# Kernel optimization log

Hardware: AMD Instinct MI355X
Metric: run time of the kernel (lower is better)

## Reference

```python
import jax, jax.numpy as jnp
import numpy as np


def setup_inputs() -> dict:
    key = jax.random.key(0)
    k1, k2, k3 = jax.random.split(key, 3)
    N, E, C_in, C_out = 100000, 3200000, 256, 64
    x = jax.random.normal(k1, (N, C_in), dtype=jnp.float32)
    edge_index = jax.random.randint(k2, (2, E), 0, N, dtype=jnp.int64)
    W = jax.random.normal(k3, (C_in, C_out), dtype=jnp.float32) * (1.0 / np.sqrt(C_in))
    b = jnp.zeros((C_out,), dtype=jnp.float32)
    return {"x": x, "edge_index": edge_index, "W": W, "b": b}


def reference(x, edge_index, W, b):
    # GCNConv: out = D^{-1/2} (A + I) D^{-1/2} (X W) + b
    N = x.shape[0]
    loop = jnp.arange(N, dtype=edge_index.dtype)
    src = jnp.concatenate([edge_index[0], loop])  # [E+N]
    dst = jnp.concatenate([edge_index[1], loop])  # [E+N]
    # degree (with self-loops) on destination nodes, unit edge weights
    deg = jax.ops.segment_sum(jnp.ones_like(dst, dtype=x.dtype), dst, num_segments=N)
    dinv = jnp.where(deg > 0, jax.lax.rsqrt(deg), 0.0)
    norm = dinv[src] * dinv[dst]  # [E+N]
    h = x @ W  # [N, C_out] dense projection before message passing
    msg = h[src] * norm[:, None]  # gather + scale
    out = jax.ops.segment_sum(msg, dst, num_segments=N)  # scatter-add
    return out + b
```

## Files before the change

### kernel.cpp

```cpp
#include <hip/hip_runtime.h>
#include <hip/hip_bf16.h>

#define CIN 256
#define COUT 64
#define WPAD 264
#define BSHIFT 7
#define NPB 128
#define NWG 1024

typedef __attribute__((ext_vector_type(8))) short short8;
typedef __attribute__((ext_vector_type(4))) float floatx4;

static __device__ __forceinline__ unsigned int fbits(float f) {
    return __builtin_bit_cast(unsigned int, f);
}
static __device__ __forceinline__ float bbits(unsigned int u) {
    return __builtin_bit_cast(float, u);
}
static __device__ __forceinline__ unsigned short f2bf(float f) {
    unsigned u = fbits(f);
    return (unsigned short)((u + 0x7FFFu + ((u >> 16) & 1u)) >> 16);
}
static __device__ __forceinline__ float bf2f(unsigned short h) {
    return bbits(((unsigned)h) << 16);
}

union U8 { short8 s; unsigned int u[4]; };
static __device__ __forceinline__ void split8(floatx4 a0, floatx4 a1,
                                              short8& hi, short8& lo) {
    float f[8] = {a0[0], a0[1], a0[2], a0[3], a1[0], a1[1], a1[2], a1[3]};
    U8 H, L;
#pragma unroll
    for (int j = 0; j < 4; ++j) {
        unsigned u0 = fbits(f[2 * j]);
        unsigned u1 = fbits(f[2 * j + 1]);
        H.u[j] = __builtin_amdgcn_perm(u1, u0, 0x07060302u);
        float r0 = f[2 * j] - bbits(u0 & 0xFFFF0000u);
        float r1 = f[2 * j + 1] - bbits(u1 & 0xFFFF0000u);
        L.u[j] = __builtin_amdgcn_perm(fbits(r1), fbits(r0), 0x07060302u);
    }
    hi = H.s;
    lo = L.s;
}

__global__ __launch_bounds__(256) void k1_bucket_hist(const int* __restrict__ dst,
                                                      int* __restrict__ H,
                                                      int E, int chunk, int nbuck) {
    __shared__ int cnt[1024];
    for (int i = threadIdx.x; i < nbuck; i += 256) cnt[i] = 0;
    __syncthreads();
    const int g = blockIdx.x;
    const int e0 = g * chunk;
    const int e1 = min(E, e0 + chunk);
    for (int e = e0 + threadIdx.x; e < e1; e += 256)
        atomicAdd(&cnt[dst[e] >> BSHIFT], 1);
    __syncthreads();
    for (int i = threadIdx.x; i < nbuck; i += 256) H[i * NWG + g] = cnt[i];
}

__global__ __launch_bounds__(1024) void scan_a(const int* __restrict__ in,
                                               int* __restrict__ out,
                                               int* __restrict__ bsums, int n) {
    __shared__ int sm[1024];
    int i = blockIdx.x * 1024 + threadIdx.x;
    int v = (i < n) ? in[i] : 0;
    sm[threadIdx.x] = v;
    __syncthreads();
    for (int off = 1; off < 1024; off <<= 1) {
        int t = (threadIdx.x >= off) ? sm[threadIdx.x - off] : 0;
        __syncthreads();
        sm[threadIdx.x] += t;
        __syncthreads();
    }
    if (i < n) out[i] = sm[threadIdx.x] - v;
    if (threadIdx.x == 1023) bsums[blockIdx.x] = sm[1023];
}

__global__ __launch_bounds__(1024) void scan_b(const int* __restrict__ bsums,
                                               int* __restrict__ boffs, int NB) {
    __shared__ int sm[1024];
    int v = (threadIdx.x < NB) ? bsums[threadIdx.x] : 0;
    sm[threadIdx.x] = v;
    __syncthreads();
    for (int off = 1; off < 1024; off <<= 1) {
        int t = (threadIdx.x >= off) ? sm[threadIdx.x - off] : 0;
        __syncthreads();
        sm[threadIdx.x] += t;
        __syncthreads();
    }
    if (threadIdx.x < NB) boffs[threadIdx.x] = sm[threadIdx.x] - v;
}

__global__ __launch_bounds__(256) void k3_bin(const int* __restrict__ src,
                                              const int* __restrict__ dst,
                                              const int* __restrict__ O,
                                              const int* __restrict__ boffs,
                                              int* __restrict__ packed,
                                              int E, int chunk, int nbuck) {
    __shared__ int cur[1024];
    const int g = blockIdx.x;
    for (int i = threadIdx.x; i < nbuck; i += 256) {
        const int fi = i * NWG + g;
        cur[i] = O[fi] + boffs[fi >> 10];
    }
    __syncthreads();
    const int e0 = g * chunk;
    const int e1 = min(E, e0 + chunk);
    for (int e = e0 + threadIdx.x; e < e1; e += 256) {
        const int d = dst[e];
        const int b = d >> BSHIFT;
        const int pos = atomicAdd(&cur[b], 1);
        packed[pos] = ((d & (NPB - 1)) << 17) | src[e];
    }
}

__global__ __launch_bounds__(256) void k4_local_sort(const int* __restrict__ O,
                                                     const int* __restrict__ boffs,
                                                     const int* __restrict__ packed,
                                                     int* __restrict__ rowptr,
                                                     float* __restrict__ dinv,
                                                     int* __restrict__ col,
                                                     int N, int E, int nbuck) {
    __shared__ int lcnt[NPB];
    __shared__ int s[NPB];
    __shared__ int lpos[NPB];
    const int b = blockIdx.x;
    const int ib = b * NWG;
    const int segbeg = O[ib] + boffs[ib >> 10];
    int segend = E;
    if (b + 1 < nbuck) {
        const int ie = (b + 1) * NWG;
        segend = O[ie] + boffs[ie >> 10];
    }
    const int n0 = b << BSHIFT;
    const int ncnt = min(N - n0, NPB);
    const int t = threadIdx.x;

    if (t < NPB) lcnt[t] = 0;
    __syncthreads();
    for (int e = segbeg + t; e < segend; e += 256)
        atomicAdd(&lcnt[packed[e] >> 17], 1);
    __syncthreads();
    if (t < NPB) s[t] = lcnt[t];
    __syncthreads();
    for (int off = 1; off < NPB; off <<= 1) {
        int v = 0;
        if (t < NPB && t >= off) v = s[t - off];
        __syncthreads();
        if (t < NPB) s[t] += v;
        __syncthreads();
    }
    if (t < NPB) {
        const int excl = s[t] - lcnt[t];
        lpos[t] = excl;
        if (t < ncnt) {
            rowptr[n0 + t] = segbeg + excl;
            dinv[n0 + t] = rsqrtf((float)(lcnt[t] + 1));
        }
    }
    if (b == nbuck - 1 && t == 0) rowptr[N] = E;
    __syncthreads();
    for (int e = segbeg + t; e < segend; e += 256) {
        const int p = packed[e];
        const int dl = p >> 17;
        const int pos = segbeg + atomicAdd(&lpos[dl], 1);
        col[pos] = p & 0x1FFFF;
    }
}

__global__ __launch_bounds__(512) void gemm_mfma_kernel(const float* __restrict__ x,
                                                        const float* __restrict__ W,
                                                        const float* __restrict__ dinv,
                                                        unsigned short* __restrict__ h2,
                                                        int N) {
    __shared__ unsigned short Whi[COUT * WPAD];
    __shared__ unsigned short Wlo[COUT * WPAD];
    for (int i = threadIdx.x; i < CIN * COUT; i += 512) {
        int k = i >> 6, c = i & 63;
        float w = W[i];
        unsigned u = fbits(w);
        unsigned short h = (unsigned short)(u >> 16);
        float r = w - bbits(u & 0xFFFF0000u);
        Whi[c * WPAD + k] = h;
        Wlo[c * WPAD + k] = (unsigned short)(fbits(r) >> 16);
    }
    __syncthreads();

    const int lane = threadIdx.x & 63;
    const int wave = threadIdx.x >> 6;
    const int m = lane & 15;
    const int q = lane >> 4;
    const int row0 = blockIdx.x * 256 + wave * 32;

    int ar0 = row0 + m;
    int ar1 = row0 + 16 + m;
    if (ar0 >= N) ar0 = N - 1;
    if (ar1 >= N) ar1 = N - 1;
    const float* __restrict__ xr0 = x + (size_t)ar0 * CIN + q * 8;
    const float* __restrict__ xr1 = x + (size_t)ar1 * CIN + q * 8;

    floatx4 acc0[4] = {floatx4{0,0,0,0}, floatx4{0,0,0,0}, floatx4{0,0,0,0}, floatx4{0,0,0,0}};
    floatx4 acc1[4] = {floatx4{0,0,0,0}, floatx4{0,0,0,0}, floatx4{0,0,0,0}, floatx4{0,0,0,0}};

#pragma unroll
    for (int kc = 0; kc < 8; ++kc) {
        floatx4 a00 = *(const floatx4*)(xr0 + kc * 32);
        floatx4 a01 = *(const floatx4*)(xr0 + kc * 32 + 4);
        floatx4 a10 = *(const floatx4*)(xr1 + kc * 32);
        floatx4 a11 = *(const floatx4*)(xr1 + kc * 32 + 4);
        short8 ahi0, alo0, ahi1, alo1;
        split8(a00, a01, ahi0, alo0);
        split8(a10, a11, ahi1, alo1);
        const int kb = kc * 32 + q * 8;
#pragma unroll
        for (int ct = 0; ct < 4; ++ct) {
            const int c = ct * 16 + m;
            short8 bhi = *(const short8*)&Whi[c * WPAD + kb];
            short8 blo = *(const short8*)&Wlo[c * WPAD + kb];
            acc0[ct] = __builtin_amdgcn_mfma_f32_16x16x32_bf16(ahi0, bhi, acc0[ct], 0, 0, 0);
            acc0[ct] = __builtin_amdgcn_mfma_f32_16x16x32_bf16(ahi0, blo, acc0[ct], 0, 0, 0);
            acc0[ct] = __builtin_amdgcn_mfma_f32_16x16x32_bf16(alo0, bhi, acc0[ct], 0, 0, 0);
            acc1[ct] = __builtin_amdgcn_mfma_f32_16x16x32_bf16(ahi1, bhi, acc1[ct], 0, 0, 0);
            acc1[ct] = __builtin_amdgcn_mfma_f32_16x16x32_bf16(ahi1, blo, acc1[ct], 0, 0, 0);
            acc1[ct] = __builtin_amdgcn_mfma_f32_16x16x32_bf16(alo1, bhi, acc1[ct], 0, 0, 0);
        }
    }

#pragma unroll
    for (int t = 0; t < 2; ++t) {
#pragma unroll
        for (int r = 0; r < 4; ++r) {
            const int row = row0 + t * 16 + q * 4 + r;
            if (row < N) {
                const float dv = dinv[row];
                unsigned short* __restrict__ op = h2 + (size_t)row * COUT;
#pragma unroll
                for (int ct = 0; ct < 4; ++ct) {
                    float v = (t == 0) ? acc0[ct][r] : acc1[ct][r];
                    op[ct * 16 + m] = f2bf(v * dv);
                }
            }
        }
    }
}

__global__ __launch_bounds__(256) void gather_kernel(const unsigned short* __restrict__ h2,
                                                     const int* __restrict__ rowptr,
                                                     const int* __restrict__ col,
                                                     const float* __restrict__ dinv,
                                                     const float* __restrict__ b,
                                                     float* __restrict__ out, int N) {
    const int lane = threadIdx.x & 63;
    const int h = lane >> 5;
    const int c = lane & 31;
    const int node = blockIdx.x * 4 + (threadIdx.x >> 6);
    if (node >= N) return;
    const unsigned* __restrict__ h2u = (const unsigned*)h2;
    const int p0 = rowptr[node];
    const int p1 = rowptr[node + 1];
    float a0 = 0.f, a1 = 0.f;
    int p = p0;

    const int nmain = (p1 - p0) >> 4;
    if (nmain > 0) {
        int e0 = col[p + h],      e1 = col[p + 2 + h];
        int e2 = col[p + 4 + h],  e3 = col[p + 6 + h];
        int e4 = col[p + 8 + h],  e5 = col[p + 10 + h];
        int e6 = col[p + 12 + h], e7 = col[p + 14 + h];
        for (int it = 0; it < nmain; ++it) {
            const unsigned u0 = h2u[(size_t)e0 * 32 + c];
            const unsigned u1 = h2u[(size_t)e1 * 32 + c];
            const unsigned u2 = h2u[(size_t)e2 * 32 + c];
            const unsigned u3 = h2u[(size_t)e3 * 32 + c];
            const unsigned u4 = h2u[(size_t)e4 * 32 + c];
            const unsigned u5 = h2u[(size_t)e5 * 32 + c];
            const unsigned u6 = h2u[(size_t)e6 * 32 + c];
            const unsigned u7 = h2u[(size_t)e7 * 32 + c];
            const int pn = p + 16;
            if (it + 1 < nmain) {
                e0 = col[pn + h];      e1 = col[pn + 2 + h];
                e2 = col[pn + 4 + h];  e3 = col[pn + 6 + h];
                e4 = col[pn + 8 + h];  e5 = col[pn + 10 + h];
                e6 = col[pn + 12 + h]; e7 = col[pn + 14 + h];
            }
            a0 += ((bbits(u0 << 16) + bbits(u1 << 16)) + (bbits(u2 << 16) + bbits(u3 << 16))) +
                  ((bbits(u4 << 16) + bbits(u5 << 16)) + (bbits(u6 << 16) + bbits(u7 << 16)));
            a1 += ((bbits(u0 & 0xFFFF0000u) + bbits(u1 & 0xFFFF0000u)) +
                   (bbits(u2 & 0xFFFF0000u) + bbits(u3 & 0xFFFF0000u))) +
                  ((bbits(u4 & 0xFFFF0000u) + bbits(u5 & 0xFFFF0000u)) +
                   (bbits(u6 & 0xFFFF0000u) + bbits(u7 & 0xFFFF0000u)));
            p = pn;
        }
    }
    for (; p + 7 < p1; p += 8) {
        const int e0 = col[p + h],     e1 = col[p + 2 + h];
        const int e2 = col[p + 4 + h], e3 = col[p + 6 + h];
        const unsigned u0 = h2u[(size_t)e0 * 32 + c];
        const unsigned u1 = h2u[(size_t)e1 * 32 + c];
        const unsigned u2 = h2u[(size_t)e2 * 32 + c];
        const unsigned u3 = h2u[(size_t)e3 * 32 + c];
        a0 += (bbits(u0 << 16) + bbits(u1 << 16)) + (bbits(u2 << 16) + bbits(u3 << 16));
        a1 += (bbits(u0 & 0xFFFF0000u) + bbits(u1 & 0xFFFF0000u)) +
              (bbits(u2 & 0xFFFF0000u) + bbits(u3 & 0xFFFF0000u));
    }
    for (; p + 1 < p1; p += 2) {
        const int e = col[p + h];
        const unsigned u = h2u[(size_t)e * 32 + c];
        a0 += bbits(u << 16);
        a1 += bbits(u & 0xFFFF0000u);
    }
    if (p < p1 && h == 0) {
        const unsigned u = h2u[(size_t)col[p] * 32 + c];
        a0 += bbits(u << 16);
        a1 += bbits(u & 0xFFFF0000u);
    }
    a0 += __shfl_xor(a0, 32, 64);
    a1 += __shfl_xor(a1, 32, 64);
    if (h == 0) {
        const unsigned su = h2u[(size_t)node * 32 + c];
        const float dv = dinv[node];
        const float2 bb = ((const float2*)b)[c];
        float2 o;
        o.x = (a0 + bbits(su << 16)) * dv + bb.x;
        o.y = (a1 + bbits(su & 0xFFFF0000u)) * dv + bb.y;
        ((float2*)out)[(size_t)node * 32 + c] = o;
    }
}

extern "C" void kernel_launch(void* const* d_in, const int* in_sizes, int n_in,
                              void* d_out, int out_size, void* d_ws, size_t ws_size,
                              hipStream_t stream) {
    const float* x = (const float*)d_in[0];
    const int* ei = (const int*)d_in[1];
    const float* W = (const float*)d_in[2];
    const float* b = (const float*)d_in[3];
    float* out = (float*)d_out;

    const int N = in_sizes[0] / CIN;
    const int E = in_sizes[1] / 2;
    const int* src = ei;
    const int* dst = ei + E;

    const int nbuck = (N + NPB - 1) >> BSHIFT;
    const int nH = nbuck * NWG;
    const int chunk = (E + NWG - 1) / NWG;
    const int NBs = (nH + 1023) / 1024;

    auto align_up = [](size_t v) { return (v + 255) & ~(size_t)255; };
    char* ws = (char*)d_ws;
    size_t off = 0;
    int* H = (int*)(ws + off);        off = align_up(off + (size_t)nH * 4);
    int* O = (int*)(ws + off);        off = align_up(off + (size_t)nH * 4);
    int* bsums = (int*)(ws + off);    off = align_up(off + (size_t)NBs * 4);
    int* boffs = (int*)(ws + off);    off = align_up(off + (size_t)NBs * 4);
    int* rowptr = (int*)(ws + off);   off = align_up(off + (size_t)(N + 1) * 4);
    float* dinv = (float*)(ws + off); off = align_up(off + (size_t)N * 4);
    int* packed = (int*)(ws + off);   off = align_up(off + (size_t)E * 4);
    int* col = (int*)(ws + off);      off = align_up(off + (size_t)E * 4);
    unsigned short* h2 = (unsigned short*)(ws + off);
    off = align_up(off + (size_t)N * COUT * 2);
    (void)ws_size;

    k1_bucket_hist<<<NWG, 256, 0, stream>>>(dst, H, E, chunk, nbuck);
    scan_a<<<NBs, 1024, 0, stream>>>(H, O, bsums, nH);
    scan_b<<<1, 1024, 0, stream>>>(bsums, boffs, NBs);
    k3_bin<<<NWG, 256, 0, stream>>>(src, dst, O, boffs, packed, E, chunk, nbuck);
    k4_local_sort<<<nbuck, 256, 0, stream>>>(O, boffs, packed, rowptr, dinv, col, N, E, nbuck);
    gemm_mfma_kernel<<<(N + 255) / 256, 512, 0, stream>>>(x, W, dinv, h2, N);
    gather_kernel<<<(N + 3) / 4, 256, 0, stream>>>(h2, rowptr, col, dinv, b, out, N);
}
```

Measured before the change: 354.3 us.

## Pad bucket slots, stage segments in LDS, sort edges in place

Cuts the binning workgroup count from 1024 to 256 and pads each (bucket, workgroup) slot to a multiple of 16 entries, filling the gaps with sentinel values. This makes the scattered writes in the binning pass more aligned. The local-sort kernel now loads each bucket segment into shared memory once and writes the sorted column indices back into the packed buffer in place. That removes the separate col array and the second global read of the segment. The gather kernel now uses per-node begin and end offsets because the padding breaks a single contiguous rowptr. The cost is extra padding traffic and a fixed shared-memory capacity (SEGCAP) that would silently truncate unusually large segments.

```diff
diff --git a/kernel.cpp b/kernel.cpp
--- a/kernel.cpp
+++ b/kernel.cpp
@@ -6,7 +6,9 @@
 #define WPAD 264
 #define BSHIFT 7
 #define NPB 128
-#define NWG 1024
+#define NWG 256
+#define SENT ((int)0x80000000u)
+#define SEGCAP 12288
 
 typedef __attribute__((ext_vector_type(8))) short short8;
 typedef __attribute__((ext_vector_type(4))) float floatx4;
@@ -20,9 +22,6 @@
 static __device__ __forceinline__ unsigned short f2bf(float f) {
     unsigned u = fbits(f);
     return (unsigned short)((u + 0x7FFFu + ((u >> 16) & 1u)) >> 16);
-}
-static __device__ __forceinline__ float bf2f(unsigned short h) {
-    return bbits(((unsigned)h) << 16);
 }
 
 union U8 { short8 s; unsigned int u[4]; };
@@ -63,7 +62,8 @@
                                                int* __restrict__ bsums, int n) {
     __shared__ int sm[1024];
     int i = blockIdx.x * 1024 + threadIdx.x;
-    int v = (i < n) ? in[i] : 0;
+    int raw = (i < n) ? in[i] : 0;
+    int v = (raw + 15) & ~15;
     sm[threadIdx.x] = v;
     __syncthreads();
     for (int off = 1; off < 1024; off <<= 1) {
@@ -77,7 +77,8 @@
 }
 
 __global__ __launch_bounds__(1024) void scan_b(const int* __restrict__ bsums,
-                                               int* __restrict__ boffs, int NB) {
+                                               int* __restrict__ boffs,
+                                               int* __restrict__ ptot, int NB) {
     __shared__ int sm[1024];
     int v = (threadIdx.x < NB) ? bsums[threadIdx.x] : 0;
     sm[threadIdx.x] = v;
@@ -89,6 +90,7 @@
         __syncthreads();
     }
     if (threadIdx.x < NB) boffs[threadIdx.x] = sm[threadIdx.x] - v;
+    if (threadIdx.x == NB - 1) ptot[0] = sm[threadIdx.x];
 }
 
 __global__ __launch_bounds__(256) void k3_bin(const int* __restrict__ src,
@@ -112,34 +114,49 @@
         const int pos = atomicAdd(&cur[b], 1);
         packed[pos] = ((d & (NPB - 1)) << 17) | src[e];
     }
+    __syncthreads();
+    for (int i = threadIdx.x; i < nbuck; i += 256) {
+        const int c = cur[i];
+        const int end = (c + 15) & ~15;
+        for (int j = c; j < end; ++j) packed[j] = SENT;
+    }
 }
 
 __global__ __launch_bounds__(256) void k4_local_sort(const int* __restrict__ O,
                                                      const int* __restrict__ boffs,
-                                                     const int* __restrict__ packed,
-                                                     int* __restrict__ rowptr,
+                                                     const int* __restrict__ ptot,
+                                                     int* __restrict__ packed,
+                                                     int* __restrict__ rowbeg,
+                                                     int* __restrict__ rowend,
                                                      float* __restrict__ dinv,
-                                                     int* __restrict__ col,
-                                                     int N, int E, int nbuck) {
+                                                     int N, int nbuck) {
+    __shared__ int sseg[SEGCAP];
     __shared__ int lcnt[NPB];
     __shared__ int s[NPB];
     __shared__ int lpos[NPB];
     const int b = blockIdx.x;
     const int ib = b * NWG;
     const int segbeg = O[ib] + boffs[ib >> 10];
-    int segend = E;
+    int segend;
     if (b + 1 < nbuck) {
         const int ie = (b + 1) * NWG;
         segend = O[ie] + boffs[ie >> 10];
-    }
+    } else {
+        segend = ptot[0];
+    }
+    int seglen = segend - segbeg;
+    if (seglen > SEGCAP) seglen = SEGCAP;
     const int n0 = b << BSHIFT;
     const int ncnt = min(N - n0, NPB);
     const int t = threadIdx.x;
 
     if (t < NPB) lcnt[t] = 0;
-    __syncthreads();
-    for (int e = segbeg + t; e < segend; e += 256)
-        atomicAdd(&lcnt[packed[e] >> 17], 1);
+    for (int i = t; i < seglen; i += 256) sseg[i] = packed[segbeg + i];
+    __syncthreads();
+    for (int i = t; i < seglen; i += 256) {
+        const int p = sseg[i];
+        if (p >= 0) atomicAdd(&lcnt[(p >> 17) & (NPB - 1)], 1);
+    }
     __syncthreads();
     if (t < NPB) s[t] = lcnt[t];
     __syncthreads();
@@ -154,17 +171,19 @@
         const int excl = s[t] - lcnt[t];
         lpos[t] = excl;
         if (t < ncnt) {
-            rowptr[n0 + t] = segbeg + excl;
+            rowbeg[n0 + t] = segbeg + excl;
+            rowend[n0 + t] = segbeg + s[t];
             dinv[n0 + t] = rsqrtf((float)(lcnt[t] + 1));
         }
     }
-    if (b == nbuck - 1 && t == 0) rowptr[N] = E;
-    __syncthreads();
-    for (int e = segbeg + t; e < segend; e += 256) {
-        const int p = packed[e];
-        const int dl = p >> 17;
-        const int pos = segbeg + atomicAdd(&lpos[dl], 1);
-        col[pos] = p & 0x1FFFF;
+    __syncthreads();
+    for (int i = t; i < seglen; i += 256) {
+        const int p = sseg[i];
+        if (p >= 0) {
+            const int dl = (p >> 17) & (NPB - 1);
+            const int pos = segbeg + atomicAdd(&lpos[dl], 1);
+            packed[pos] = p & 0x1FFFF;
+        }
     }
 }
 
@@ -245,7 +264,8 @@
 }
 
 __global__ __launch_bounds__(256) void gather_kernel(const unsigned short* __restrict__ h2,
-                                                     const int* __restrict__ rowptr,
+                                                     const int* __restrict__ rowbeg,
+                                                     const int* __restrict__ rowend,
                                                      const int* __restrict__ col,
                                                      const float* __restrict__ dinv,
                                                      const float* __restrict__ b,
@@ -256,8 +276,8 @@
     const int node = blockIdx.x * 4 + (threadIdx.x >> 6);
     if (node >= N) return;
     const unsigned* __restrict__ h2u = (const unsigned*)h2;
-    const int p0 = rowptr[node];
-    const int p1 = rowptr[node + 1];
+    const int p0 = rowbeg[node];
+    const int p1 = rowend[node];
     float a0 = 0.f, a1 = 0.f;
     int p = p0;
 
@@ -345,6 +365,7 @@
     const int nH = nbuck * NWG;
     const int chunk = (E + NWG - 1) / NWG;
     const int NBs = (nH + 1023) / 1024;
+    const int padcap = E + 16 * nH;
 
     auto align_up = [](size_t v) { return (v + 255) & ~(size_t)255; };
     char* ws = (char*)d_ws;
@@ -353,19 +374,20 @@
     int* O = (int*)(ws + off);        off = align_up(off + (size_t)nH * 4);
     int* bsums = (int*)(ws + off);    off = align_up(off + (size_t)NBs * 4);
     int* boffs = (int*)(ws + off);    off = align_up(off + (size_t)NBs * 4);
-    int* rowptr = (int*)(ws + off);   off = align_up(off + (size_t)(N + 1) * 4);
+    int* ptot = (int*)(ws + off);     off = align_up(off + 4);
+    int* rowbeg = (int*)(ws + off);   off = align_up(off + (size_t)N * 4);
+    int* rowend = (int*)(ws + off);   off = align_up(off + (size_t)N * 4);
     float* dinv = (float*)(ws + off); off = align_up(off + (size_t)N * 4);
-    int* packed = (int*)(ws + off);   off = align_up(off + (size_t)E * 4);
-    int* col = (int*)(ws + off);      off = align_up(off + (size_t)E * 4);
+    int* packed = (int*)(ws + off);   off = align_up(off + (size_t)padcap * 4);
     unsigned short* h2 = (unsigned short*)(ws + off);
     off = align_up(off + (size_t)N * COUT * 2);
     (void)ws_size;
 
     k1_bucket_hist<<<NWG, 256, 0, stream>>>(dst, H, E, chunk, nbuck);
     scan_a<<<NBs, 1024, 0, stream>>>(H, O, bsums, nH);
-    scan_b<<<1, 1024, 0, stream>>>(bsums, boffs, NBs);
+    scan_b<<<1, 1024, 0, stream>>>(bsums, boffs, ptot, NBs);
     k3_bin<<<NWG, 256, 0, stream>>>(src, dst, O, boffs, packed, E, chunk, nbuck);
-    k4_local_sort<<<nbuck, 256, 0, stream>>>(O, boffs, packed, rowptr, dinv, col, N, E, nbuck);
+    k4_local_sort<<<nbuck, 256, 0, stream>>>(O, boffs, ptot, packed, rowbeg, rowend, dinv, N, nbuck);
     gemm_mfma_kernel<<<(N + 255) / 256, 512, 0, stream>>>(x, W, dinv, h2, N);
-    gather_kernel<<<(N + 3) / 4, 256, 0, stream>>>(h2, rowptr, col, dinv, b, out, N);
-}
+    gather_kernel<<<(N + 3) / 4, 256, 0, stream>>>(h2, rowbeg, rowend, packed, dinv, b, out, N);
+}
```

After: 387.4 us. +9.4%, slower.
